# Kernel tuning notes

Measured on AMD Instinct MI355X. Metric: run time of the kernel, lower is better.

The kernel has to match this reference:

```python
import jax, jax.numpy as jnp
import numpy as np
from jax import lax

B = 64


def _conv_bn_relu(x, w, cb, s, t):
    # 3x3 conv pad=1 (SAME), eval-mode BN folded to per-channel scale s / shift t, ReLU
    y = lax.conv_general_dilated(x, w, (1, 1), 'SAME',
                                 dimension_numbers=('NCHW', 'OIHW', 'NCHW'))
    y = y + cb[None, :, None, None]
    y = y * s[None, :, None, None] + t[None, :, None, None]
    return jax.nn.relu(y)


def _maxpool(x, k):
    return lax.reduce_window(x, -jnp.inf, lax.max, (1, 1, k, k), (1, 1, k, k), 'VALID')


def _tensor_dlt(H4PT, CornerA):
    # Batched version of the per-sample 8x8 DLT solve (faithful to the original row layout)
    U = CornerA[:, 0::2]            # [B,4]
    V = CornerA[:, 1::2]
    Ud = U + H4PT[:, 0::2]
    Vd = V + H4PT[:, 1::2]
    z = jnp.zeros_like(U)
    o = jnp.ones_like(U)
    r0 = jnp.stack([z, z, z, -U, V, -o, Vd * U, Vd * V], axis=-1)   # [B,4,8]
    r1 = jnp.stack([U, V, o, z, z, z, -Ud * U, -Ud * V], axis=-1)   # [B,4,8]
    A = jnp.stack([r0, r1], axis=2).reshape(U.shape[0], 8, 8)        # interleave rows per point
    bvec = jnp.stack([-Vd, Ud], axis=2).reshape(U.shape[0], 8)
    h = jnp.linalg.solve(A, bvec[..., None])[..., 0]                 # [B,8]
    H = jnp.concatenate([h, jnp.ones((U.shape[0], 1), h.dtype)], axis=1)
    return H.reshape(-1, 3, 3)


def _bilinear_sample(img, xs, ys):
    # img [Hs,Ws]; xs, ys [Ho,Wo]; zeros padding outside (grid_sample semantics)
    Hs, Ws = img.shape
    x0 = jnp.floor(xs)
    y0 = jnp.floor(ys)
    wx = xs - x0
    wy = ys - y0
    x0i = x0.astype(jnp.int32)
    y0i = y0.astype(jnp.int32)

    def gat(yi, xi):
        valid = (xi >= 0) & (xi < Ws) & (yi >= 0) & (yi < Hs)
        v = img[jnp.clip(yi, 0, Hs - 1), jnp.clip(xi, 0, Ws - 1)]
        return jnp.where(valid, v, jnp.zeros((), img.dtype))

    v00 = gat(y0i, x0i)
    v01 = gat(y0i, x0i + 1)
    v10 = gat(y0i + 1, x0i)
    v11 = gat(y0i + 1, x0i + 1)
    return (v00 * (1 - wx) * (1 - wy) + v01 * wx * (1 - wy)
            + v10 * (1 - wx) * wy + v11 * wx * wy)


def _warp_perspective(imgs, Hm, out_hw=(128, 128)):
    # dst(x,y) = src(H^{-1} [x,y,1]); align_corners=True pixel coordinates
    Ho, Wo = out_hw
    dt = imgs.dtype
    ys, xs = jnp.meshgrid(jnp.arange(Ho, dtype=dt), jnp.arange(Wo, dtype=dt), indexing='ij')
    grid = jnp.stack([xs, ys, jnp.ones_like(xs)], axis=-1)           # [Ho,Wo,3]
    Hinv = jnp.linalg.inv(Hm)                                        # [B,3,3]
    pts = jnp.einsum('bij,hwj->bhwi', Hinv, grid)                    # [B,Ho,Wo,3]
    xs_s = pts[..., 0] / pts[..., 2]
    ys_s = pts[..., 1] / pts[..., 2]
    out = jax.vmap(_bilinear_sample)(imgs, xs_s, ys_s)               # [B,Ho,Wo]
    return out[:, None]                                              # [B,1,Ho,Wo]


def setup_inputs() -> dict:
    key = jax.random.key(0)
    ks = jax.random.split(key, 64)
    d = {}
    d['TCropABatch'] = jax.random.uniform(ks[0], (B, 128, 128), jnp.float32)
    d['TI1Batch'] = jax.random.uniform(ks[1], (B, 2, 128, 128), jnp.float32)
    d['TImgABatch'] = jax.random.uniform(ks[2], (B, 240, 320), jnp.float32)
    # corners of a 128x128 quad inside the 240x320 image: (x,y) per corner, 8 values
    x0 = jax.random.uniform(ks[3], (B,), jnp.float32, 0.0, 192.0)
    y0 = jax.random.uniform(ks[4], (B,), jnp.float32, 0.0, 112.0)
    d['TCornerBatch'] = jnp.stack(
        [x0, y0, x0 + 127.0, y0, x0, y0 + 127.0, x0 + 127.0, y0 + 127.0], axis=1)
    chans = [(2, 64), (64, 64), (64, 64), (64, 64), (64, 128), (128, 128), (128, 128), (128, 128)]
    ki = 5
    for i, (ci, co) in enumerate(chans, start=1):
        fan = ci * 9
        d[f'w{i}'] = jax.random.normal(ks[ki], (co, ci, 3, 3), jnp.float32) * np.float32((2.0 / fan) ** 0.5)
        d[f'cb{i}'] = jnp.zeros((co,), jnp.float32)
        d[f's{i}'] = jnp.ones((co,), jnp.float32) + 0.01 * jax.random.normal(ks[ki + 1], (co,), jnp.float32)
        d[f't{i}'] = 0.01 * jax.random.normal(ks[ki + 2], (co,), jnp.float32)
        ki += 3
    d['fcw'] = jax.random.normal(ks[ki], (1024, 512), jnp.float32) * 0.02
    d['fcb'] = jnp.zeros((1024,), jnp.float32)
    d['f1w'] = jax.random.normal(ks[ki + 1], (8, 1024), jnp.float32) * 0.01
    d['f1b'] = jnp.zeros((8,), jnp.float32)
    return d


def reference(TCropABatch, TI1Batch, TImgABatch, TCornerBatch,
              w1, cb1, s1, t1, w2, cb2, s2, t2, w3, cb3, s3, t3, w4, cb4, s4, t4,
              w5, cb5, s5, t5, w6, cb6, s6, t6, w7, cb7, s7, t7, w8, cb8, s8, t8,
              fcw, fcb, f1w, f1b):
    ws = [w1, w2, w3, w4, w5, w6, w7, w8]
    cbs = [cb1, cb2, cb3, cb4, cb5, cb6, cb7, cb8]
    ss = [s1, s2, s3, s4, s5, s6, s7, s8]
    ts = [t1, t2, t3, t4, t5, t6, t7, t8]
    pools = [None, 2, None, 2, None, 2, None, 6]
    out = TI1Batch
    for i in range(8):
        out = _conv_bn_relu(out, ws[i], cbs[i], ss[i], ts[i])
        if pools[i] is not None:
            out = _maxpool(out, pools[i])
    out = out.reshape(out.shape[0], -1)                 # [B,512]
    out = jax.nn.relu(out @ fcw.T + fcb)                # dropout is eval-mode identity
    H4PT = out @ f1w.T + f1b                            # [B,8]
    Hm = _tensor_dlt(H4PT, TCornerBatch)                # [B,3,3]
    b_Pred = _warp_perspective(TImgABatch, Hm)          # [B,1,128,128]
    return b_Pred
```

## Files before the change

### kernel.cpp

```cpp
#include <hip/hip_runtime.h>
#include <math.h>

typedef __attribute__((ext_vector_type(4))) float f32x4;
typedef __attribute__((ext_vector_type(8))) short sh8;

__device__ __forceinline__ float bf2f(unsigned short u){
    union { unsigned int i; float f; } v; v.i = ((unsigned)u) << 16; return v.f;
}
__device__ __forceinline__ unsigned short f2bf(float f){
    union { float f; unsigned int i; } v; v.f = f;
    unsigned int x = v.i;
    x += 0x7fff + ((x >> 16) & 1);
    return (unsigned short)(x >> 16);
}

struct WTArgs {
    const float* src[7];
    unsigned short* hi[7];
    int cin[7];
    int start[8];
};

__global__ void wtrans_all(WTArgs a)
{
    int e = blockIdx.x * 256 + threadIdx.x;
    if (e >= a.start[7]) return;
    int l = 0;
    while (e >= a.start[l + 1]) l++;
    int eL = e - a.start[l];
    int CIN = a.cin[l];
    int tap = eL % 9, rest = eL / 9;
    int ci = rest % CIN, co = rest / CIN;
    int COUT = (a.start[l + 1] - a.start[l]) / (9 * CIN);
    a.hi[l][(tap * COUT + co) * CIN + ci] = f2bf(a.src[l][eL]);
}

__global__ __launch_bounds__(256) void conv1_kernel(
    const float* __restrict__ in, const float* __restrict__ w,
    const float* __restrict__ cb, const float* __restrict__ sc,
    const float* __restrict__ tb, unsigned short* __restrict__ out)
{
    __shared__ float s_w[18 * 64];
    __shared__ float s_in[2][18 * 20];

    const int tid = threadIdx.x;
    const int b = blockIdx.y;
    const int tile = blockIdx.x;
    const int ty = tile >> 3, tx = tile & 7;
    const int y0 = ty * 16, x0 = tx * 16;

    for (int idx = tid; idx < 1152; idx += 256) {
        int co = idx & 63, kk2 = idx >> 6;
        s_w[kk2 * 64 + co] = w[co * 18 + kk2];
    }
    for (int idx = tid; idx < 2 * 324; idx += 256) {
        int ci = idx / 324, rem = idx % 324;
        int r = rem / 18, c = rem % 18;
        int gy = y0 + r - 1, gx = x0 + c - 1;
        float v = 0.f;
        if (gy >= 0 && gy < 128 && gx >= 0 && gx < 128)
            v = in[((size_t)(b * 2 + ci) * 128 + gy) * 128 + gx];
        s_in[ci][r * 20 + c] = v;
    }
    __syncthreads();

    const int cog = tid >> 5;
    const int slot = tid & 31;
    const int sy = slot >> 2, sx = slot & 3;

    float p[2][4][6];
#pragma unroll
    for (int ci = 0; ci < 2; ci++)
#pragma unroll
        for (int r = 0; r < 4; r++)
#pragma unroll
            for (int c = 0; c < 6; c++)
                p[ci][r][c] = s_in[ci][(2 * sy + r) * 20 + 4 * sx + c];

    float acc[2][4][8];
#pragma unroll
    for (int r = 0; r < 2; r++)
#pragma unroll
        for (int c = 0; c < 4; c++)
#pragma unroll
            for (int o = 0; o < 8; o++) acc[r][c][o] = 0.f;

#pragma unroll
    for (int kk2 = 0; kk2 < 18; kk2++) {
        const int ci = kk2 / 9, k = kk2 % 9;
        const int ky = k / 3, kx = k % 3;
        float wv[8];
#pragma unroll
        for (int q = 0; q < 2; q++) {
            f32x4 w4 = *(const f32x4*)(&s_w[kk2 * 64 + cog * 8 + q * 4]);
#pragma unroll
            for (int z = 0; z < 4; z++) wv[q * 4 + z] = w4[z];
        }
#pragma unroll
        for (int r = 0; r < 2; r++)
#pragma unroll
            for (int c = 0; c < 4; c++) {
                float pv = p[ci][r + ky][c + kx];
#pragma unroll
                for (int o = 0; o < 8; o++) acc[r][c][o] += pv * wv[o];
            }
    }

    float bb[8], ss[8], tt[8];
#pragma unroll
    for (int o = 0; o < 8; o++) { bb[o] = cb[cog*8+o]; ss[o] = sc[cog*8+o]; tt[o] = tb[cog*8+o]; }
#pragma unroll
    for (int r = 0; r < 2; r++)
#pragma unroll
        for (int c = 0; c < 4; c++) {
            unsigned short ov[8];
#pragma unroll
            for (int o = 0; o < 8; o++)
                ov[o] = f2bf(fmaxf((acc[r][c][o] + bb[o]) * ss[o] + tt[o], 0.f));
            int py = y0 + 2 * sy + r, px = x0 + 4 * sx + c;
            *(sh8*)(out + ((size_t)(b * 128 + py) * 128 + px) * 64 + cog * 8) = *(sh8*)ov;
        }
}

template<int CIN, int COUT, int HI, int WI, int POOL, int TW>
__global__ __launch_bounds__(256, 2) void conv_mfma(
    const unsigned short* __restrict__ in,
    const unsigned short* __restrict__ whi,
    const float* __restrict__ cb, const float* __restrict__ sc,
    const float* __restrict__ tb, unsigned short* __restrict__ out)
{
    constexpr int TH = 256 / TW;
    constexpr int HALW = TW + 2, HALH = TH + 2;
    constexpr int NPIX = HALW * HALH;
    constexpr int CHUNKS = CIN / 64;
    constexpr int TILESX = WI / TW;
    constexpr int HO = HI / POOL, WO = WI / POOL;
    constexpr int ST = 68;

    __shared__ __align__(16) unsigned short lds_A[NPIX * ST];
    __shared__ __align__(16) unsigned short lds_W[2][4096];

    const int tid = threadIdx.x;
    const int lane = tid & 63;
    const int i = lane & 15, j = lane >> 4;
    const int wv = tid >> 6;
    const int tile = blockIdx.x;
    const int ty = tile / TILESX, tx = tile % TILESX;
    const int y0 = ty * TH, x0 = tx * TW;
    const int coBase = blockIdx.y * 64;
    const int b = blockIdx.z;

    const int co_s = tid >> 2;
    const int gp = tid & 3;

    f32x4 acc[4][4];
#pragma unroll
    for (int pf = 0; pf < 4; pf++)
#pragma unroll
        for (int cf = 0; cf < 4; cf++) acc[pf][cf] = (f32x4){0.f, 0.f, 0.f, 0.f};

    sh8 rw[2];

    for (int c = 0; c < CHUNKS; c++) {
        if (c) __syncthreads();

        for (int u = tid; u < NPIX * 8; u += 256) {
            int hp = u >> 3, c16 = u & 7;
            int hy = hp / HALW, hx = hp % HALW;
            int gy = y0 + hy - 1, gx = x0 + hx - 1;
            sh8 v = (sh8){0,0,0,0,0,0,0,0};
            if (gy >= 0 && gy < HI && gx >= 0 && gx < WI)
                v = *(const sh8*)(in + ((size_t)(b * HI + gy) * WI + gx) * CIN + c * 64 + c16 * 8);
            *(sh8*)(&lds_A[hp * ST + c16 * 8]) = v;
        }

        const unsigned short* wrow = whi + ((size_t)(coBase + co_s)) * CIN + c * 64;

        auto LOADW = [&](int tap) {
#pragma unroll
            for (int q = 0; q < 2; q++) {
                int pp = gp + q * 4;
                int gl = pp ^ (co_s & 7);
                rw[q] = *(const sh8*)(wrow + (size_t)tap * COUT * CIN + gl * 8);
            }
        };
        auto WRITEW = [&](int bi) {
#pragma unroll
            for (int q = 0; q < 2; q++) {
                int pp = gp + q * 4;
                *(sh8*)(&lds_W[bi][co_s * 64 + pp * 8]) = rw[q];
            }
        };

        LOADW(0); WRITEW(0);
        __syncthreads();

#pragma unroll
        for (int tap = 0; tap < 9; tap++) {
            if (tap < 8) LOADW(tap + 1);
            const int ky = tap / 3, kx = tap % 3;
            const int bi = tap & 1;
            sh8 aF[8], bF[8];
#pragma unroll
            for (int kk = 0; kk < 2; kk++) {
#pragma unroll
                for (int pf = 0; pf < 4; pf++) {
                    const int nf = wv * 4 + pf;
                    int hy2, hx2;
                    if (TW == 32) { hy2 = (nf >> 1) + ky; hx2 = (nf & 1) * 16 + i + kx; }
                    else          { hy2 = nf + ky;        hx2 = i + kx; }
                    aF[kk * 4 + pf] = *(const sh8*)(&lds_A[(hy2 * HALW + hx2) * ST + kk * 32 + j * 8]);
                }
#pragma unroll
                for (int cf = 0; cf < 4; cf++) {
                    const int co_l = cf * 16 + i;
                    bF[kk * 4 + cf] = *(const sh8*)(&lds_W[bi][co_l * 64
                        + ((((kk << 2) | j) ^ (i & 7)) * 8)]);
                }
            }
            __builtin_amdgcn_s_setprio(1);
#pragma unroll
            for (int kk = 0; kk < 2; kk++)
#pragma unroll
                for (int pf = 0; pf < 4; pf++)
#pragma unroll
                    for (int cf = 0; cf < 4; cf++)
                        acc[pf][cf] = __builtin_amdgcn_mfma_f32_16x16x32_bf16(
                            aF[kk * 4 + pf], bF[kk * 4 + cf], acc[pf][cf], 0, 0, 0);
            __builtin_amdgcn_s_setprio(0);
            if (tap < 8) { WRITEW((tap + 1) & 1); __syncthreads(); }
        }
    }

#pragma unroll
    for (int cf = 0; cf < 4; cf++) {
        const int co = coBase + cf * 16 + i;
        const float b3 = cb[co], s3 = sc[co], t3 = tb[co];
        if (POOL == 1) {
#pragma unroll
            for (int pf = 0; pf < 4; pf++) {
                const int nf = wv * 4 + pf;
                int py, pxb;
                if (TW == 32) { py = nf >> 1; pxb = (nf & 1) * 16; }
                else          { py = nf;      pxb = 0; }
#pragma unroll
                for (int r = 0; r < 4; r++) {
                    float v = fmaxf((acc[pf][cf][r] + b3) * s3 + t3, 0.f);
                    int px = pxb + j * 4 + r;
                    out[((size_t)(b * HO + y0 + py) * WO + x0 + px) * COUT + co] = f2bf(v);
                }
            }
        } else if constexpr (POOL == 2 && TW == 32) {
#pragma unroll
            for (int h = 0; h < 2; h++) {
                const int pfA = h, pfB = 2 + h;
#pragma unroll
                for (int r2 = 0; r2 < 2; r2++) {
                    float vA0 = fmaxf((acc[pfA][cf][2*r2]   + b3) * s3 + t3, 0.f);
                    float vA1 = fmaxf((acc[pfA][cf][2*r2+1] + b3) * s3 + t3, 0.f);
                    float vB0 = fmaxf((acc[pfB][cf][2*r2]   + b3) * s3 + t3, 0.f);
                    float vB1 = fmaxf((acc[pfB][cf][2*r2+1] + b3) * s3 + t3, 0.f);
                    float v = fmaxf(fmaxf(vA0, vA1), fmaxf(vB0, vB1));
                    int pox = (x0 >> 1) + h * 8 + j * 2 + r2;
                    int poy = (y0 >> 1) + wv;
                    out[((size_t)(b * HO + poy) * WO + pox) * COUT + co] = f2bf(v);
                }
            }
        }
    }
}

__global__ void pool6_kernel(const unsigned short* __restrict__ in, float* __restrict__ out)
{
    int t = blockIdx.x * 256 + threadIdx.x;
    if (t >= 64 * 128 * 4) return;
    int ox = t & 1, oy = (t >> 1) & 1, c = (t >> 2) & 127, b = t >> 9;
    const unsigned short* p = in + ((size_t)(b * 16 + oy * 6) * 16 + ox * 6) * 128 + c;
    float m = -INFINITY;
#pragma unroll
    for (int r = 0; r < 6; r++)
#pragma unroll
        for (int cc = 0; cc < 6; cc++) m = fmaxf(m, bf2f(p[(r * 16 + cc) * 128]));
    out[(size_t)b * 512 + c * 4 + oy * 2 + ox] = m;
}

__global__ void fc1_kernel(const float* __restrict__ flat, const float* __restrict__ fcw,
                           const float* __restrict__ fcb, float* __restrict__ out1)
{
    int b = blockIdx.y;
    int jj = blockIdx.x * 256 + threadIdx.x;
    const f32x4* f = (const f32x4*)(flat + (size_t)b * 512);
    const f32x4* w = (const f32x4*)(fcw + (size_t)jj * 512);
    float s = fcb[jj];
    for (int k = 0; k < 128; k++) {
        f32x4 a = f[k], ww = w[k];
        s += a[0]*ww[0] + a[1]*ww[1] + a[2]*ww[2] + a[3]*ww[3];
    }
    out1[(size_t)b * 1024 + jj] = fmaxf(s, 0.f);
}

__global__ void fc2_kernel(const float* __restrict__ out1, const float* __restrict__ f1w,
                           const float* __restrict__ f1b, float* __restrict__ h4pt)
{
    int b = blockIdx.x;
    int o = threadIdx.x >> 5, s2 = threadIdx.x & 31;
    const float* pa = out1 + (size_t)b * 1024;
    const float* pw = f1w + (size_t)o * 1024;
    float s = 0.f;
    for (int k = s2; k < 1024; k += 32) s += pa[k] * pw[k];
#pragma unroll
    for (int m = 16; m; m >>= 1) s += __shfl_xor(s, m);
    if (s2 == 0) h4pt[b * 8 + o] = s + f1b[o];
}

__global__ void dlt_kernel(const float* __restrict__ h4pt, const float* __restrict__ corner,
                           double* __restrict__ hinv)
{
    int b = threadIdx.x;
    if (b >= 64) return;
    double U[4], V[4], Ud[4], Vd[4];
    for (int jq = 0; jq < 4; jq++) {
        U[jq] = (double)corner[b * 8 + 2 * jq];
        V[jq] = (double)corner[b * 8 + 2 * jq + 1];
        Ud[jq] = U[jq] + (double)h4pt[b * 8 + 2 * jq];
        Vd[jq] = V[jq] + (double)h4pt[b * 8 + 2 * jq + 1];
    }
    double A[8][9];
    for (int jq = 0; jq < 4; jq++) {
        double* r0 = A[2 * jq];
        double* r1 = A[2 * jq + 1];
        r0[0] = 0;     r0[1] = 0;     r0[2] = 0;
        r0[3] = -U[jq]; r0[4] = V[jq]; r0[5] = -1;
        r0[6] = Vd[jq] * U[jq]; r0[7] = Vd[jq] * V[jq]; r0[8] = -Vd[jq];
        r1[0] = U[jq]; r1[1] = V[jq]; r1[2] = 1;
        r1[3] = 0;     r1[4] = 0;     r1[5] = 0;
        r1[6] = -Ud[jq] * U[jq]; r1[7] = -Ud[jq] * V[jq]; r1[8] = Ud[jq];
    }
    for (int col = 0; col < 8; col++) {
        int piv = col; double mx = fabs(A[col][col]);
        for (int r = col + 1; r < 8; r++) {
            double v = fabs(A[r][col]);
            if (v > mx) { mx = v; piv = r; }
        }
        if (piv != col)
            for (int cc = col; cc < 9; cc++) { double tmp = A[col][cc]; A[col][cc] = A[piv][cc]; A[piv][cc] = tmp; }
        double inv = 1.0 / A[col][col];
        for (int r = col + 1; r < 8; r++) {
            double f = A[r][col] * inv;
            for (int cc = col; cc < 9; cc++) A[r][cc] -= f * A[col][cc];
        }
    }
    double h[9];
    for (int r = 7; r >= 0; r--) {
        double s = A[r][8];
        for (int cc = r + 1; cc < 8; cc++) s -= A[r][cc] * h[cc];
        h[r] = s / A[r][r];
    }
    h[8] = 1.0;
    double a = h[0], bb = h[1], cq = h[2], d = h[3], e = h[4], f = h[5], g = h[6], hh = h[7], iq = h[8];
    double C00 = e * iq - f * hh, C01 = cq * hh - bb * iq, C02 = bb * f - cq * e;
    double C10 = f * g - d * iq,  C11 = a * iq - cq * g,   C12 = cq * d - a * f;
    double C20 = d * hh - e * g,  C21 = bb * g - a * hh,   C22 = a * e - bb * d;
    double det = a * C00 + bb * C10 + cq * C20;
    double idet = 1.0 / det;
    double* o = hinv + b * 9;
    o[0] = C00 * idet; o[1] = C01 * idet; o[2] = C02 * idet;
    o[3] = C10 * idet; o[4] = C11 * idet; o[5] = C12 * idet;
    o[6] = C20 * idet; o[7] = C21 * idet; o[8] = C22 * idet;
}

__global__ void warp_kernel(const float* __restrict__ img, const double* __restrict__ hinv,
                            float* __restrict__ out)
{
    int b = blockIdx.y;
    int pix = blockIdx.x * 256 + threadIdx.x;
    int y = pix >> 7, x = pix & 127;
    const double* h = hinv + b * 9;
    double X = (double)x, Y = (double)y;
    double p0 = h[0] * X + h[1] * Y + h[2];
    double p1 = h[3] * X + h[4] * Y + h[5];
    double p2 = h[6] * X + h[7] * Y + h[8];
    double xs = p0 / p2, ys = p1 / p2;
    double x0d = floor(xs), y0d = floor(ys);
    double wx = xs - x0d, wy = ys - y0d;
    int x0 = (int)x0d, y0 = (int)y0d;
    const float* im = img + (size_t)b * 240 * 320;
    auto gat = [&](int yi, int xi) -> double {
        bool valid = (xi >= 0) & (xi < 320) & (yi >= 0) & (yi < 240);
        int yc = yi < 0 ? 0 : (yi > 239 ? 239 : yi);
        int xc = xi < 0 ? 0 : (xi > 319 ? 319 : xi);
        double v = (double)im[yc * 320 + xc];
        return valid ? v : 0.0;
    };
    double v00 = gat(y0, x0),     v01 = gat(y0, x0 + 1);
    double v10 = gat(y0 + 1, x0), v11 = gat(y0 + 1, x0 + 1);
    double r = v00 * (1 - wx) * (1 - wy) + v01 * wx * (1 - wy)
             + v10 * (1 - wx) * wy       + v11 * wx * wy;
    out[((size_t)b << 14) + pix] = (float)r;
}

extern "C" void kernel_launch(void* const* d_in, const int* in_sizes, int n_in,
                              void* d_out, int out_size, void* d_ws, size_t ws_size,
                              hipStream_t stream)
{
    const float* TI1     = (const float*)d_in[1];
    const float* TImgA   = (const float*)d_in[2];
    const float* TCorner = (const float*)d_in[3];
    const float* w[8], *cbp[8], *sp[8], *tp[8];
    for (int l = 0; l < 8; l++) {
        w[l]   = (const float*)d_in[4 + 4 * l];
        cbp[l] = (const float*)d_in[5 + 4 * l];
        sp[l]  = (const float*)d_in[6 + 4 * l];
        tp[l]  = (const float*)d_in[7 + 4 * l];
    }
    const float* fcw = (const float*)d_in[36];
    const float* fcb = (const float*)d_in[37];
    const float* f1w = (const float*)d_in[38];
    const float* f1b = (const float*)d_in[39];

    char* base = (char*)d_ws;
    unsigned short* A    = (unsigned short*)(base);
    unsigned short* Bb   = (unsigned short*)(base + 33554432);
    unsigned short* whiA = (unsigned short*)(base + 67108864);
    float*  feat = (float*) (base + 67108864 + 1253376);
    float*  fc1o = feat + 64 * 512;
    float*  h4pt = fc1o + 64 * 1024;
    double* hinv = (double*)(h4pt + 512);
    float*  outp = (float*)d_out;

    const int CINS[7]  = {64, 64, 64, 64, 128, 128, 128};
    const int COUTS[7] = {64, 64, 64, 128, 128, 128, 128};
    int wofs[8]; wofs[0] = 0;
    for (int l = 0; l < 7; l++) wofs[l + 1] = wofs[l] + 9 * COUTS[l] * CINS[l];

    WTArgs wa;
    for (int l = 0; l < 7; l++) {
        wa.src[l] = w[l + 1];
        wa.hi[l] = whiA + wofs[l];
        wa.cin[l] = CINS[l];
        wa.start[l] = wofs[l];
    }
    wa.start[7] = wofs[7];
    wtrans_all<<<(wofs[7] + 255) / 256, 256, 0, stream>>>(wa);

    for (int ch = 0; ch < 4; ch++) {
        conv1_kernel<<<dim3(64, 16), 256, 0, stream>>>(
            TI1 + (size_t)ch * 16 * 2 * 128 * 128, w[0], cbp[0], sp[0], tp[0], A);
        conv_mfma<64, 64, 128, 128, 2, 32><<<dim3(64, 1, 16), 256, 0, stream>>>(
            A, whiA + wofs[0], cbp[1], sp[1], tp[1],
            Bb + (size_t)ch * 16 * 64 * 64 * 64);
    }
    conv_mfma<64, 64, 64, 64, 1, 32><<<dim3(16, 1, 64), 256, 0, stream>>>(
        Bb, whiA + wofs[1], cbp[2], sp[2], tp[2], A);
    conv_mfma<64, 64, 64, 64, 2, 32><<<dim3(16, 1, 64), 256, 0, stream>>>(
        A, whiA + wofs[2], cbp[3], sp[3], tp[3], Bb);
    conv_mfma<64, 128, 32, 32, 1, 32><<<dim3(4, 2, 64), 256, 0, stream>>>(
        Bb, whiA + wofs[3], cbp[4], sp[4], tp[4], A);
    conv_mfma<128, 128, 32, 32, 2, 32><<<dim3(4, 2, 64), 256, 0, stream>>>(
        A, whiA + wofs[4], cbp[5], sp[5], tp[5], Bb);
    conv_mfma<128, 128, 16, 16, 1, 16><<<dim3(1, 2, 64), 256, 0, stream>>>(
        Bb, whiA + wofs[5], cbp[6], sp[6], tp[6], A);
    conv_mfma<128, 128, 16, 16, 1, 16><<<dim3(1, 2, 64), 256, 0, stream>>>(
        A, whiA + wofs[6], cbp[7], sp[7], tp[7], Bb);

    pool6_kernel<<<128, 256, 0, stream>>>(Bb, feat);
    fc1_kernel<<<dim3(4, 64), 256, 0, stream>>>(feat, fcw, fcb, fc1o);
    fc2_kernel<<<64, 256, 0, stream>>>(fc1o, f1w, f1b, h4pt);
    dlt_kernel<<<1, 64, 0, stream>>>(h4pt, TCorner, hinv);
    warp_kernel<<<dim3(64, 64), 256, 0, stream>>>(TImgA, hinv, outp);
}
```

Before: 387.5 us.

## Parametrize conv output-channel tile and batch weight taps per sync stage

```diff
diff --git a/kernel.cpp b/kernel.cpp
--- a/kernel.cpp
+++ b/kernel.cpp
@@ -122,10 +122,10 @@
         }
 }
 
-template<int CIN, int COUT, int HI, int WI, int POOL, int TW>
+template<int CIN, int COUT, int HI, int WI, int POOL, int TW, int CF, int TPB>
 __global__ __launch_bounds__(256, 2) void conv_mfma(
     const unsigned short* __restrict__ in,
-    const unsigned short* __restrict__ whi,
+    const unsigned short* __restrict__ wgt,
     const float* __restrict__ cb, const float* __restrict__ sc,
     const float* __restrict__ tb, unsigned short* __restrict__ out)
 {
@@ -136,9 +136,12 @@
     constexpr int TILESX = WI / TW;
     constexpr int HO = HI / POOL, WO = WI / POOL;
     constexpr int ST = 68;
+    constexpr int NCO = CF * 16;
+    constexpr int NP = (9 + TPB - 1) / TPB;
+    constexpr int WBUF = TPB * NCO * 64;
 
     __shared__ __align__(16) unsigned short lds_A[NPIX * ST];
-    __shared__ __align__(16) unsigned short lds_W[2][4096];
+    __shared__ __align__(16) unsigned short lds_W[2][WBUF];
 
     const int tid = threadIdx.x;
     const int lane = tid & 63;
@@ -147,19 +150,16 @@
     const int tile = blockIdx.x;
     const int ty = tile / TILESX, tx = tile % TILESX;
     const int y0 = ty * TH, x0 = tx * TW;
-    const int coBase = blockIdx.y * 64;
+    const int coBase = blockIdx.y * NCO;
     const int b = blockIdx.z;
 
-    const int co_s = tid >> 2;
-    const int gp = tid & 3;
-
-    f32x4 acc[4][4];
+    f32x4 acc[4][CF];
 #pragma unroll
     for (int pf = 0; pf < 4; pf++)
 #pragma unroll
-        for (int cf = 0; cf < 4; cf++) acc[pf][cf] = (f32x4){0.f, 0.f, 0.f, 0.f};
-
-    sh8 rw[2];
+        for (int cf = 0; cf < CF; cf++) acc[pf][cf] = (f32x4){0.f, 0.f, 0.f, 0.f};
+
+    sh8 rw[4];
 
     for (int c = 0; c < CHUNKS; c++) {
         if (c) __syncthreads();
@@ -174,66 +174,70 @@
             *(sh8*)(&lds_A[hp * ST + c16 * 8]) = v;
         }
 
-        const unsigned short* wrow = whi + ((size_t)(coBase + co_s)) * CIN + c * 64;
-
-        auto LOADW = [&](int tap) {
-#pragma unroll
-            for (int q = 0; q < 2; q++) {
-                int pp = gp + q * 4;
-                int gl = pp ^ (co_s & 7);
-                rw[q] = *(const sh8*)(wrow + (size_t)tap * COUT * CIN + gl * 8);
+        auto LOADW = [&](int p) {
+            const int tap0 = p * TPB;
+#pragma unroll
+            for (int q = 0; q < 4; q++) {
+                int g = tid + q * 256;
+                int slot = g & 7;
+                int co = (g >> 3) & (NCO - 1);
+                int t = (TPB == 2) ? (g >> 9) : 0;
+                int tap = tap0 + t; if (tap > 8) tap = 8;
+                int gl = slot ^ (co & 7);
+                rw[q] = *(const sh8*)(wgt + ((size_t)(tap * COUT + coBase + co)) * CIN
+                                      + c * 64 + gl * 8);
             }
         };
         auto WRITEW = [&](int bi) {
 #pragma unroll
-            for (int q = 0; q < 2; q++) {
-                int pp = gp + q * 4;
-                *(sh8*)(&lds_W[bi][co_s * 64 + pp * 8]) = rw[q];
-            }
+            for (int q = 0; q < 4; q++)
+                *(sh8*)(&lds_W[bi][(tid + q * 256) * 8]) = rw[q];
         };
 
         LOADW(0); WRITEW(0);
         __syncthreads();
 
 #pragma unroll
-        for (int tap = 0; tap < 9; tap++) {
-            if (tap < 8) LOADW(tap + 1);
-            const int ky = tap / 3, kx = tap % 3;
-            const int bi = tap & 1;
-            sh8 aF[8], bF[8];
-#pragma unroll
-            for (int kk = 0; kk < 2; kk++) {
-#pragma unroll
-                for (int pf = 0; pf < 4; pf++) {
-                    const int nf = wv * 4 + pf;
-                    int hy2, hx2;
-                    if (TW == 32) { hy2 = (nf >> 1) + ky; hx2 = (nf & 1) * 16 + i + kx; }
-                    else          { hy2 = nf + ky;        hx2 = i + kx; }
-                    aF[kk * 4 + pf] = *(const sh8*)(&lds_A[(hy2 * HALW + hx2) * ST + kk * 32 + j * 8]);
-                }
-#pragma unroll
-                for (int cf = 0; cf < 4; cf++) {
-                    const int co_l = cf * 16 + i;
-                    bF[kk * 4 + cf] = *(const sh8*)(&lds_W[bi][co_l * 64
-                        + ((((kk << 2) | j) ^ (i & 7)) * 8)]);
+        for (int p = 0; p < NP; p++) {
+            if (p + 1 < NP) LOADW(p + 1);
+            const int bi = p & 1;
+#pragma unroll
+            for (int t = 0; t < TPB; t++) {
+                const int tap = p * TPB + t;
+                if (tap > 8) continue;
+                const int ky = tap / 3, kx = tap % 3;
+#pragma unroll
+                for (int kk = 0; kk < 2; kk++) {
+                    sh8 aF[4], bF[CF];
+#pragma unroll
+                    for (int pf = 0; pf < 4; pf++) {
+                        const int nf = wv * 4 + pf;
+                        int hy2, hx2;
+                        if (TW == 32) { hy2 = (nf >> 1) + ky; hx2 = (nf & 1) * 16 + i + kx; }
+                        else          { hy2 = nf + ky;        hx2 = i + kx; }
+                        aF[pf] = *(const sh8*)(&lds_A[(hy2 * HALW + hx2) * ST + kk * 32 + j * 8]);
+                    }
+#pragma unroll
+                    for (int cf = 0; cf < CF; cf++) {
+                        const int phys = ((kk << 2) | j) ^ (i & 7);
+                        bF[cf] = *(const sh8*)(&lds_W[bi][((t * NCO + cf * 16 + i) * 8 + phys) * 8]);
+                    }
+                    __builtin_amdgcn_s_setprio(1);
+#pragma unroll
+                    for (int pf = 0; pf < 4; pf++)
+#pragma unroll
+                        for (int cf = 0; cf < CF; cf++)
+                            acc[pf][cf] = __builtin_amdgcn_mfma_f32_16x16x32_bf16(
+                                aF[pf], bF[cf], acc[pf][cf], 0, 0, 0);
+                    __builtin_amdgcn_s_setprio(0);
                 }
             }
-            __builtin_amdgcn_s_setprio(1);
-#pragma unroll
-            for (int kk = 0; kk < 2; kk++)
-#pragma unroll
-                for (int pf = 0; pf < 4; pf++)
-#pragma unroll
-                    for (int cf = 0; cf < 4; cf++)
-                        acc[pf][cf] = __builtin_amdgcn_mfma_f32_16x16x32_bf16(
-                            aF[kk * 4 + pf], bF[kk * 4 + cf], acc[pf][cf], 0, 0, 0);
-            __builtin_amdgcn_s_setprio(0);
-            if (tap < 8) { WRITEW((tap + 1) & 1); __syncthreads(); }
-        }
-    }
-
-#pragma unroll
-    for (int cf = 0; cf < 4; cf++) {
+            if (p + 1 < NP) { WRITEW((p + 1) & 1); __syncthreads(); }
+        }
+    }
+
+#pragma unroll
+    for (int cf = 0; cf < CF; cf++) {
         const int co = coBase + cf * 16 + i;
         const float b3 = cb[co], s3 = sc[co], t3 = tb[co];
         if (POOL == 1) {
@@ -446,21 +450,21 @@
     for (int ch = 0; ch < 4; ch++) {
         conv1_kernel<<<dim3(64, 16), 256, 0, stream>>>(
             TI1 + (size_t)ch * 16 * 2 * 128 * 128, w[0], cbp[0], sp[0], tp[0], A);
-        conv_mfma<64, 64, 128, 128, 2, 32><<<dim3(64, 1, 16), 256, 0, stream>>>(
+        conv_mfma<64, 64, 128, 128, 2, 32, 4, 2><<<dim3(64, 1, 16), 256, 0, stream>>>(
             A, whiA + wofs[0], cbp[1], sp[1], tp[1],
             Bb + (size_t)ch * 16 * 64 * 64 * 64);
     }
-    conv_mfma<64, 64, 64, 64, 1, 32><<<dim3(16, 1, 64), 256, 0, stream>>>(
+    conv_mfma<64, 64, 64, 64, 1, 32, 4, 2><<<dim3(16, 1, 64), 256, 0, stream>>>(
         Bb, whiA + wofs[1], cbp[2], sp[2], tp[2], A);
-    conv_mfma<64, 64, 64, 64, 2, 32><<<dim3(16, 1, 64), 256, 0, stream>>>(
+    conv_mfma<64, 64, 64, 64, 2, 32, 4, 2><<<dim3(16, 1, 64), 256, 0, stream>>>(
         A, whiA + wofs[2], cbp[3], sp[3], tp[3], Bb);
-    conv_mfma<64, 128, 32, 32, 1, 32><<<dim3(4, 2, 64), 256, 0, stream>>>(
+    conv_mfma<64, 128, 32, 32, 1, 32, 8, 1><<<dim3(4, 1, 64), 256, 0, stream>>>(
         Bb, whiA + wofs[3], cbp[4], sp[4], tp[4], A);
-    conv_mfma<128, 128, 32, 32, 2, 32><<<dim3(4, 2, 64), 256, 0, stream>>>(
+    conv_mfma<128, 128, 32, 32, 2, 32, 8, 1><<<dim3(4, 1, 64), 256, 0, stream>>>(
         A, whiA + wofs[4], cbp[5], sp[5], tp[5], Bb);
-    conv_mfma<128, 128, 16, 16, 1, 16><<<dim3(1, 2, 64), 256, 0, stream>>>(
+    conv_mfma<128, 128, 16, 16, 1, 16, 4, 2><<<dim3(1, 2, 64), 256, 0, stream>>>(
         Bb, whiA + wofs[5], cbp[6], sp[6], tp[6], A);
-    conv_mfma<128, 128, 16, 16, 1, 16><<<dim3(1, 2, 64), 256, 0, stream>>>(
+    conv_mfma<128, 128, 16, 16, 1, 16, 4, 2><<<dim3(1, 2, 64), 256, 0, stream>>>(
         A, whiA + wofs[6], cbp[7], sp[7], tp[7], Bb);
 
     pool6_kernel<<<128, 256, 0, stream>>>(Bb, feat);
```

After: 400.8 us. 3.4% more time.

## Split MFMA conv waves across output channels and add K-split for last layers

Applied to the files above, without the earlier changes.

```diff
diff --git a/kernel.cpp b/kernel.cpp
--- a/kernel.cpp
+++ b/kernel.cpp
@@ -122,20 +122,24 @@
         }
 }
 
-template<int CIN, int COUT, int HI, int WI, int POOL, int TW>
-__global__ __launch_bounds__(256, 2) void conv_mfma(
+template<int CIN, int COUT, int HI, int WI, int POOL, int TW, int NPG, int KSPLIT>
+__global__ __launch_bounds__(NPG * 128, 4) void conv_mfma(
     const unsigned short* __restrict__ in,
-    const unsigned short* __restrict__ whi,
+    const unsigned short* __restrict__ wgt,
     const float* __restrict__ cb, const float* __restrict__ sc,
-    const float* __restrict__ tb, unsigned short* __restrict__ out)
-{
-    constexpr int TH = 256 / TW;
+    const float* __restrict__ tb, void* __restrict__ outv)
+{
+    constexpr int THREADS = NPG * 128;
+    constexpr int TH = (TW == 32) ? 2 * NPG : 4 * NPG;
     constexpr int HALW = TW + 2, HALH = TH + 2;
     constexpr int NPIX = HALW * HALH;
     constexpr int CHUNKS = CIN / 64;
     constexpr int TILESX = WI / TW;
     constexpr int HO = HI / POOL, WO = WI / POOL;
     constexpr int ST = 68;
+    constexpr int NCOG = COUT / 64;
+    constexpr int GPT = 512 / THREADS;
+    constexpr int LOG_NPG = (NPG == 4) ? 2 : 1;
 
     __shared__ __align__(16) unsigned short lds_A[NPIX * ST];
     __shared__ __align__(16) unsigned short lds_W[2][4096];
@@ -144,27 +148,30 @@
     const int lane = tid & 63;
     const int i = lane & 15, j = lane >> 4;
     const int wv = tid >> 6;
+    const int pg = wv & (NPG - 1);
+    const int cg = wv >> LOG_NPG;
     const int tile = blockIdx.x;
     const int ty = tile / TILESX, tx = tile % TILESX;
     const int y0 = ty * TH, x0 = tx * TW;
-    const int coBase = blockIdx.y * 64;
+    const int cogrp = (NCOG == 1) ? 0 : (blockIdx.y & (NCOG - 1));
+    const int kc = (KSPLIT == 2) ? (blockIdx.y >> (NCOG == 2 ? 1 : 0)) : 0;
+    const int coBase = cogrp * 64;
     const int b = blockIdx.z;
 
-    const int co_s = tid >> 2;
-    const int gp = tid & 3;
-
-    f32x4 acc[4][4];
+    f32x4 acc[4][2];
 #pragma unroll
     for (int pf = 0; pf < 4; pf++)
 #pragma unroll
-        for (int cf = 0; cf < 4; cf++) acc[pf][cf] = (f32x4){0.f, 0.f, 0.f, 0.f};
-
-    sh8 rw[2];
-
-    for (int c = 0; c < CHUNKS; c++) {
-        if (c) __syncthreads();
-
-        for (int u = tid; u < NPIX * 8; u += 256) {
+        for (int cf = 0; cf < 2; cf++) acc[pf][cf] = (f32x4){0.f, 0.f, 0.f, 0.f};
+
+    sh8 rw[GPT];
+
+    constexpr int NCH = (KSPLIT == 2) ? 1 : CHUNKS;
+    for (int cc = 0; cc < NCH; cc++) {
+        const int c = (KSPLIT == 2) ? kc : cc;
+        if (cc) __syncthreads();
+
+        for (int u = tid; u < NPIX * 8; u += THREADS) {
             int hp = u >> 3, c16 = u & 7;
             int hy = hp / HALW, hx = hp % HALW;
             int gy = y0 + hy - 1, gx = x0 + hx - 1;
@@ -174,22 +181,21 @@
             *(sh8*)(&lds_A[hp * ST + c16 * 8]) = v;
         }
 
-        const unsigned short* wrow = whi + ((size_t)(coBase + co_s)) * CIN + c * 64;
-
         auto LOADW = [&](int tap) {
 #pragma unroll
-            for (int q = 0; q < 2; q++) {
-                int pp = gp + q * 4;
-                int gl = pp ^ (co_s & 7);
-                rw[q] = *(const sh8*)(wrow + (size_t)tap * COUT * CIN + gl * 8);
+            for (int q = 0; q < GPT; q++) {
+                int g = tid + q * THREADS;
+                int slot = g & 7;
+                int co = g >> 3;
+                int gl = slot ^ (co & 7);
+                rw[q] = *(const sh8*)(wgt + ((size_t)(tap * COUT + coBase + co)) * CIN
+                                      + c * 64 + gl * 8);
             }
         };
         auto WRITEW = [&](int bi) {
 #pragma unroll
-            for (int q = 0; q < 2; q++) {
-                int pp = gp + q * 4;
-                *(sh8*)(&lds_W[bi][co_s * 64 + pp * 8]) = rw[q];
-            }
+            for (int q = 0; q < GPT; q++)
+                *(sh8*)(&lds_W[bi][(tid + q * THREADS) * 8]) = rw[q];
         };
 
         LOADW(0); WRITEW(0);
@@ -200,54 +206,72 @@
             if (tap < 8) LOADW(tap + 1);
             const int ky = tap / 3, kx = tap % 3;
             const int bi = tap & 1;
-            sh8 aF[8], bF[8];
 #pragma unroll
             for (int kk = 0; kk < 2; kk++) {
+                sh8 aF[4], bF[2];
 #pragma unroll
                 for (int pf = 0; pf < 4; pf++) {
-                    const int nf = wv * 4 + pf;
+                    const int nf = pg * 4 + pf;
                     int hy2, hx2;
                     if (TW == 32) { hy2 = (nf >> 1) + ky; hx2 = (nf & 1) * 16 + i + kx; }
                     else          { hy2 = nf + ky;        hx2 = i + kx; }
-                    aF[kk * 4 + pf] = *(const sh8*)(&lds_A[(hy2 * HALW + hx2) * ST + kk * 32 + j * 8]);
+                    aF[pf] = *(const sh8*)(&lds_A[(hy2 * HALW + hx2) * ST + kk * 32 + j * 8]);
                 }
 #pragma unroll
-                for (int cf = 0; cf < 4; cf++) {
-                    const int co_l = cf * 16 + i;
-                    bF[kk * 4 + cf] = *(const sh8*)(&lds_W[bi][co_l * 64
-                        + ((((kk << 2) | j) ^ (i & 7)) * 8)]);
+                for (int cf = 0; cf < 2; cf++) {
+                    const int co_l = cg * 32 + cf * 16 + i;
+                    const int phys = ((kk << 2) | j) ^ (co_l & 7);
+                    bF[cf] = *(const sh8*)(&lds_W[bi][(co_l * 8 + phys) * 8]);
                 }
+                __builtin_amdgcn_s_setprio(1);
+#pragma unroll
+                for (int pf = 0; pf < 4; pf++)
+#pragma unroll
+                    for (int cf = 0; cf < 2; cf++)
+                        acc[pf][cf] = __builtin_amdgcn_mfma_f32_16x16x32_bf16(
+                            aF[pf], bF[cf], acc[pf][cf], 0, 0, 0);
+                __builtin_amdgcn_s_setprio(0);
             }
-            __builtin_amdgcn_s_setprio(1);
-#pragma unroll
-            for (int kk = 0; kk < 2; kk++)
-#pragma unroll
-                for (int pf = 0; pf < 4; pf++)
-#pragma unroll
-                    for (int cf = 0; cf < 4; cf++)
-                        acc[pf][cf] = __builtin_amdgcn_mfma_f32_16x16x32_bf16(
-                            aF[kk * 4 + pf], bF[kk * 4 + cf], acc[pf][cf], 0, 0, 0);
-            __builtin_amdgcn_s_setprio(0);
             if (tap < 8) { WRITEW((tap + 1) & 1); __syncthreads(); }
         }
     }
 
-#pragma unroll
-    for (int cf = 0; cf < 4; cf++) {
-        const int co = coBase + cf * 16 + i;
-        const float b3 = cb[co], s3 = sc[co], t3 = tb[co];
-        if (POOL == 1) {
+    if constexpr (KSPLIT == 2) {
+        float* po = (float*)outv + (size_t)kc * 64 * HO * WO * COUT;
+#pragma unroll
+        for (int cf = 0; cf < 2; cf++) {
+            const int co = coBase + cg * 32 + cf * 16 + i;
 #pragma unroll
             for (int pf = 0; pf < 4; pf++) {
-                const int nf = wv * 4 + pf;
+                const int nf = pg * 4 + pf;
                 int py, pxb;
                 if (TW == 32) { py = nf >> 1; pxb = (nf & 1) * 16; }
                 else          { py = nf;      pxb = 0; }
 #pragma unroll
+                for (int r = 0; r < 4; r++)
+                    po[((size_t)(b * HO + y0 + py) * WO + x0 + pxb + j * 4 + r) * COUT + co] =
+                        acc[pf][cf][r];
+            }
+        }
+        return;
+    }
+
+    unsigned short* out = (unsigned short*)outv;
+#pragma unroll
+    for (int cf = 0; cf < 2; cf++) {
+        const int co = coBase + cg * 32 + cf * 16 + i;
+        const float b3 = cb[co], s3 = sc[co], t3 = tb[co];
+        if (POOL == 1) {
+#pragma unroll
+            for (int pf = 0; pf < 4; pf++) {
+                const int nf = pg * 4 + pf;
+                int py, pxb;
+                if (TW == 32) { py = nf >> 1; pxb = (nf & 1) * 16; }
+                else          { py = nf;      pxb = 0; }
+#pragma unroll
                 for (int r = 0; r < 4; r++) {
                     float v = fmaxf((acc[pf][cf][r] + b3) * s3 + t3, 0.f);
-                    int px = pxb + j * 4 + r;
-                    out[((size_t)(b * HO + y0 + py) * WO + x0 + px) * COUT + co] = f2bf(v);
+                    out[((size_t)(b * HO + y0 + py) * WO + x0 + pxb + j * 4 + r) * COUT + co] = f2bf(v);
                 }
             }
         } else if constexpr (POOL == 2 && TW == 32) {
@@ -262,12 +286,22 @@
                     float vB1 = fmaxf((acc[pfB][cf][2*r2+1] + b3) * s3 + t3, 0.f);
                     float v = fmaxf(fmaxf(vA0, vA1), fmaxf(vB0, vB1));
                     int pox = (x0 >> 1) + h * 8 + j * 2 + r2;
-                    int poy = (y0 >> 1) + wv;
+                    int poy = (y0 >> 1) + pg;
                     out[((size_t)(b * HO + poy) * WO + pox) * COUT + co] = f2bf(v);
                 }
             }
         }
     }
+}
+
+__global__ void combine_k(const float* __restrict__ part, const float* __restrict__ cb,
+                          const float* __restrict__ sc, const float* __restrict__ tb,
+                          unsigned short* __restrict__ out)
+{
+    int e = blockIdx.x * 256 + threadIdx.x;
+    int co = e & 127;
+    float v = part[e] + part[e + 2097152];
+    out[e] = f2bf(fmaxf((v + cb[co]) * sc[co] + tb[co], 0.f));
 }
 
 __global__ void pool6_kernel(const unsigned short* __restrict__ in, float* __restrict__ out)
@@ -428,6 +462,11 @@
     double* hinv = (double*)(h4pt + 512);
     float*  outp = (float*)d_out;
 
+    float*          part7   = (float*)A;
+    unsigned short* c7out   = (unsigned short*)(base + 33554432 + 8388608);
+    float*          part8   = (float*)A;
+    unsigned short* c8out   = (unsigned short*)(base + 33554432 + 16777216);
+
     const int CINS[7]  = {64, 64, 64, 64, 128, 128, 128};
     const int COUTS[7] = {64, 64, 64, 128, 128, 128, 128};
     int wofs[8]; wofs[0] = 0;
@@ -446,24 +485,26 @@
     for (int ch = 0; ch < 4; ch++) {
         conv1_kernel<<<dim3(64, 16), 256, 0, stream>>>(
             TI1 + (size_t)ch * 16 * 2 * 128 * 128, w[0], cbp[0], sp[0], tp[0], A);
-        conv_mfma<64, 64, 128, 128, 2, 32><<<dim3(64, 1, 16), 256, 0, stream>>>(
+        conv_mfma<64, 64, 128, 128, 2, 32, 4, 1><<<dim3(64, 1, 16), 512, 0, stream>>>(
             A, whiA + wofs[0], cbp[1], sp[1], tp[1],
             Bb + (size_t)ch * 16 * 64 * 64 * 64);
     }
-    conv_mfma<64, 64, 64, 64, 1, 32><<<dim3(16, 1, 64), 256, 0, stream>>>(
+    conv_mfma<64, 64, 64, 64, 1, 32, 4, 1><<<dim3(16, 1, 64), 512, 0, stream>>>(
         Bb, whiA + wofs[1], cbp[2], sp[2], tp[2], A);
-    conv_mfma<64, 64, 64, 64, 2, 32><<<dim3(16, 1, 64), 256, 0, stream>>>(
+    conv_mfma<64, 64, 64, 64, 2, 32, 4, 1><<<dim3(16, 1, 64), 512, 0, stream>>>(
         A, whiA + wofs[2], cbp[3], sp[3], tp[3], Bb);
-    conv_mfma<64, 128, 32, 32, 1, 32><<<dim3(4, 2, 64), 256, 0, stream>>>(
+    conv_mfma<64, 128, 32, 32, 1, 32, 4, 1><<<dim3(4, 2, 64), 512, 0, stream>>>(
         Bb, whiA + wofs[3], cbp[4], sp[4], tp[4], A);
-    conv_mfma<128, 128, 32, 32, 2, 32><<<dim3(4, 2, 64), 256, 0, stream>>>(
+    conv_mfma<128, 128, 32, 32, 2, 32, 4, 1><<<dim3(4, 2, 64), 512, 0, stream>>>(
         A, whiA + wofs[4], cbp[5], sp[5], tp[5], Bb);
-    conv_mfma<128, 128, 16, 16, 1, 16><<<dim3(1, 2, 64), 256, 0, stream>>>(
-        Bb, whiA + wofs[5], cbp[6], sp[6], tp[6], A);
-    conv_mfma<128, 128, 16, 16, 1, 16><<<dim3(1, 2, 64), 256, 0, stream>>>(
-        A, whiA + wofs[6], cbp[7], sp[7], tp[7], Bb);
-
-    pool6_kernel<<<128, 256, 0, stream>>>(Bb, feat);
+    conv_mfma<128, 128, 16, 16, 1, 16, 2, 2><<<dim3(2, 4, 64), 256, 0, stream>>>(
+        Bb, whiA + wofs[5], cbp[6], sp[6], tp[6], part7);
+    combine_k<<<8192, 256, 0, stream>>>(part7, cbp[6], sp[6], tp[6], c7out);
+    conv_mfma<128, 128, 16, 16, 1, 16, 2, 2><<<dim3(2, 4, 64), 256, 0, stream>>>(
+        c7out, whiA + wofs[6], cbp[7], sp[7], tp[7], part8);
+    combine_k<<<8192, 256, 0, stream>>>(part8, cbp[7], sp[7], tp[7], c8out);
+
+    pool6_kernel<<<128, 256, 0, stream>>>(c8out, feat);
     fc1_kernel<<<dim3(4, 64), 256, 0, stream>>>(feat, fcw, fcb, fc1o);
     fc2_kernel<<<64, 256, 0, stream>>>(fc1o, f1w, f1b, h4pt);
     dlt_kernel<<<1, 64, 0, stream>>>(h4pt, TCorner, hinv);
```

Result: faster. 367.5 us (-5.2%).
